# Kernel optimization log

Hardware: AMD Instinct MI355X
Metric: run time of the kernel (lower is better)

The kernel has to match this reference:

```python
import jax, jax.numpy as jnp
import numpy as np

D_MODEL = 256
SELF_NHEAD = 8
ATT_NHEAD = 8
DFF = 1024
H2D, W2D = 40, 40
MAX_DIS = 7
WS = 2 * MAX_DIS + 1  # 15x15 local window
LOCAL_DIL = 1
GN_GROUPS = 32
EPS = 1e-5


def _ln(x, g, b):
    m = jnp.mean(x, -1, keepdims=True)
    v = jnp.var(x, -1, keepdims=True)
    return (x - m) * jax.lax.rsqrt(v + EPS) * g + b


def _mha_core(q, k, v, nh):
    # q,k,v: (L, B, C); Q scaled by 1/sqrt(head_dim) as in AOT MultiheadAttention
    Lq, B, C = q.shape
    hd = C // nh
    qh = (q / jnp.asarray(hd ** 0.5, q.dtype)).reshape(Lq, B, nh, hd).transpose(1, 2, 0, 3)
    kh = k.reshape(-1, B, nh, hd).transpose(1, 2, 0, 3)
    vh = v.reshape(-1, B, nh, hd).transpose(1, 2, 0, 3)
    attn = jax.nn.softmax(jnp.einsum('bhqd,bhkd->bhqk', qh, kh), axis=-1)
    o = jnp.einsum('bhqk,bhkd->bhqd', attn, vh)
    return o.transpose(2, 0, 1, 3).reshape(Lq, B, C)


def _unfold(x, ws, dil):
    # x: (N, C, H, W) -> (N, C, ws*ws, H, W) local windows (zero-padded)
    n, c, h, w = x.shape
    p = (ws // 2) * dil
    pat = jax.lax.conv_general_dilated_patches(
        x, (ws, ws), (1, 1), [(p, p), (p, p)], rhs_dilation=(dil, dil))
    return pat.reshape(n, c, ws * ws, h, w)


def _local_attn(q2, k2, v2, nh, ws, dil):
    # q2,k2,v2: (B, C, H, W); windowed attention over (2*max_dis+1)^2 neighborhood
    b, c, h, w = q2.shape
    hd = c // nh
    qh = (q2 / jnp.asarray(hd ** 0.5, q2.dtype)).reshape(b, nh, hd, h * w)
    uk = _unfold(k2, ws, dil).reshape(b, nh, hd, ws * ws, h * w)
    uv = _unfold(v2, ws, dil).reshape(b, nh, hd, ws * ws, h * w)
    valid = _unfold(jnp.ones((1, 1, h, w), q2.dtype), ws, dil).reshape(1, 1, ws * ws, h * w) > 0.5
    logits = jnp.einsum('bhdn,bhdwn->bhwn', qh, uk)
    logits = jnp.where(valid, logits, jnp.asarray(-1e9, logits.dtype))
    attn = jax.nn.softmax(logits, axis=2)
    o = jnp.einsum('bhwn,bhdwn->bhdn', attn, uv)
    return o.reshape(b, c, h * w).transpose(2, 0, 1)  # (HW, B, C)


def _seq_to_2d(x, h, w):
    l, b, c = x.shape
    return x.reshape(h, w, b, c).transpose(2, 3, 0, 1)  # (B, C, h, w)


def _block(tgt, curr_id_emb, self_pos,
           ln1_g, ln1_b, sa_wq, sa_bq, sa_wk, sa_bk, sa_wv, sa_bv, sa_wo, sa_bo,
           ln2_g, ln2_b, w_qv, b_qv, w_id, b_id, lt_wo, lt_bo, st_wo, st_bo,
           ln3_g, ln3_b, w1, b1, gn_g, gn_b, dw_k, w2, b2):
    h, w = H2D, W2D
    # --- self attention (global_dilation == 1) ---
    _t = _ln(tgt, ln1_g, ln1_b)
    qk_in = _t + self_pos
    q_ = qk_in @ sa_wq.T + sa_bq
    k_ = qk_in @ sa_wk.T + sa_bk
    v_ = _t @ sa_wv.T + sa_bv
    tgt2 = _mha_core(q_, k_, v_, SELF_NHEAD) @ sa_wo.T + sa_bo
    tgt = tgt + tgt2
    # --- QV projection + ID-gated KV fusion ---
    _t = _ln(tgt, ln2_g, ln2_b)
    qv = _t @ w_qv.T + b_qv
    curr_Q = qv[..., :D_MODEL]  # curr_K == curr_Q
    curr_V = qv[..., D_MODEL:]
    id_kv = curr_id_emb @ w_id.T + b_id
    id_k = id_kv[..., :ATT_NHEAD]
    id_v = id_kv[..., ATT_NHEAD:]
    L, B, C = curr_Q.shape
    hd = C // ATT_NHEAD
    global_K = (curr_Q.reshape(L, B, ATT_NHEAD, hd) * (1.0 + jnp.tanh(id_k))[..., None]).reshape(L, B, C)
    global_V = curr_V + id_v
    # --- long-term (global) attention, no input linear ---
    tgt2 = _mha_core(curr_Q, global_K, global_V, ATT_NHEAD) @ lt_wo.T + lt_bo
    # --- short-term (local windowed) attention ---
    lq = _seq_to_2d(curr_Q, h, w)
    lk = _seq_to_2d(global_K, h, w)
    lv = _seq_to_2d(global_V, h, w)
    tgt3 = _local_attn(lq, lk, lv, ATT_NHEAD, WS, LOCAL_DIL) @ st_wo.T + st_bo
    tgt = tgt + tgt2 + tgt3
    # --- FFN with GN + GELU + depthwise 5x5 conv (GNActDWConv2d) ---
    _t = _ln(tgt, ln3_g, ln3_b)
    x = _t @ w1.T + b1  # (L, B, DFF)
    x2 = _seq_to_2d(x, h, w)  # (B, DFF, h, w)
    xr = x2.reshape(B, GN_GROUPS, DFF // GN_GROUPS, h, w)
    m = xr.mean((2, 3, 4), keepdims=True)
    va = xr.var((2, 3, 4), keepdims=True)
    x2 = ((xr - m) * jax.lax.rsqrt(va + EPS)).reshape(B, DFF, h, w)
    x2 = x2 * gn_g[None, :, None, None] + gn_b[None, :, None, None]
    x2 = jax.nn.gelu(x2, approximate=False)
    x2 = jax.lax.conv_general_dilated(
        x2, dw_k, (1, 1), [(2, 2), (2, 2)], feature_group_count=DFF,
        dimension_numbers=('NCHW', 'OIHW', 'NCHW'))
    x = x2.reshape(B, DFF, h * w).transpose(2, 0, 1)
    tgt2 = x @ w2.T + b2
    return tgt + tgt2


def setup_inputs() -> dict:
    key = jax.random.key(0)
    ks = jax.random.split(key, 40)
    L = H2D * W2D
    B = 1
    C = D_MODEL
    w = lambda k, s: jax.random.normal(k, s, jnp.float32) * 0.02
    inp = {
        'tgt': jax.random.normal(ks[0], (L, B, C), jnp.float32),
        'curr_id_emb': jax.random.normal(ks[1], (L, B, C), jnp.float32),
        'self_pos': jax.random.normal(ks[2], (L, B, C), jnp.float32),
        'ln1_g': jnp.ones((C,), jnp.float32), 'ln1_b': jnp.zeros((C,), jnp.float32),
        'sa_wq': w(ks[3], (C, C)), 'sa_bq': jnp.zeros((C,), jnp.float32),
        'sa_wk': w(ks[4], (C, C)), 'sa_bk': jnp.zeros((C,), jnp.float32),
        'sa_wv': w(ks[5], (C, C)), 'sa_bv': jnp.zeros((C,), jnp.float32),
        'sa_wo': w(ks[6], (C, C)), 'sa_bo': jnp.zeros((C,), jnp.float32),
        'ln2_g': jnp.ones((C,), jnp.float32), 'ln2_b': jnp.zeros((C,), jnp.float32),
        'w_qv': w(ks[7], (2 * C, C)), 'b_qv': jnp.zeros((2 * C,), jnp.float32),
        'w_id': w(ks[8], (C + ATT_NHEAD, C)), 'b_id': jnp.zeros((C + ATT_NHEAD,), jnp.float32),
        'lt_wo': w(ks[9], (C, C)), 'lt_bo': jnp.zeros((C,), jnp.float32),
        'st_wo': w(ks[10], (C, C)), 'st_bo': jnp.zeros((C,), jnp.float32),
        'ln3_g': jnp.ones((C,), jnp.float32), 'ln3_b': jnp.zeros((C,), jnp.float32),
        'w1': w(ks[11], (DFF, C)), 'b1': jnp.zeros((DFF,), jnp.float32),
        'gn_g': jnp.ones((DFF,), jnp.float32), 'gn_b': jnp.zeros((DFF,), jnp.float32),
        'dw_k': w(ks[12], (DFF, 1, 5, 5)),
        'w2': w(ks[13], (C, DFF)), 'b2': jnp.zeros((C,), jnp.float32),
    }
    return inp


def reference(tgt, curr_id_emb, self_pos,
              ln1_g, ln1_b, sa_wq, sa_bq, sa_wk, sa_bk, sa_wv, sa_bv, sa_wo, sa_bo,
              ln2_g, ln2_b, w_qv, b_qv, w_id, b_id, lt_wo, lt_bo, st_wo, st_bo,
              ln3_g, ln3_b, w1, b1, gn_g, gn_b, dw_k, w2, b2):
    return _block(tgt, curr_id_emb, self_pos,
                  ln1_g, ln1_b, sa_wq, sa_bq, sa_wk, sa_bk, sa_wv, sa_bv, sa_wo, sa_bo,
                  ln2_g, ln2_b, w_qv, b_qv, w_id, b_id, lt_wo, lt_bo, st_wo, st_bo,
                  ln3_g, ln3_b, w1, b1, gn_g, gn_b, dw_k, w2, b2)
```

## Files before the change

### kernel.cpp

```cpp
#include <hip/hip_runtime.h>
#include <math.h>

#define L_SEQ 1600
#define CDIM 256
#define NH 8
#define HD 32
#define GRID_H 40
#define GRID_W 40
#define DFF_ 1024
#define SCALE_QK 0.17677669529663687f

typedef __attribute__((ext_vector_type(8))) short short8;
typedef __attribute__((ext_vector_type(4))) float f32x4;

__device__ __forceinline__ float waveReduceSum(float v) {
#pragma unroll
    for (int off = 32; off > 0; off >>= 1) v += __shfl_down(v, off, 64);
    return v;
}
__device__ __forceinline__ float blockReduceSum(float v, float* sh4) {
    v = waveReduceSum(v);
    int lane = threadIdx.x & 63, wid = threadIdx.x >> 6;
    __syncthreads();
    if (lane == 0) sh4[wid] = v;
    __syncthreads();
    return sh4[0] + sh4[1] + sh4[2] + sh4[3];
}

__device__ __forceinline__ unsigned short f2bf(float x) {
    union { float f; unsigned u; } v; v.f = x;
    unsigned r = (v.u + 0x7FFFu + ((v.u >> 16) & 1u)) >> 16;
    return (unsigned short)r;
}
__device__ __forceinline__ unsigned pkbf(float lo, float hi) {
    return (unsigned)f2bf(lo) | ((unsigned)f2bf(hi) << 16);
}

__global__ __launch_bounds__(256) void ln_kernel(const float* __restrict__ x,
                                                 const float* __restrict__ g,
                                                 const float* __restrict__ b,
                                                 const float* __restrict__ addin,
                                                 float* __restrict__ out,
                                                 float* __restrict__ out2) {
    __shared__ float sh4[4];
    int row = blockIdx.x;
    int c = threadIdx.x;
    float v = x[row * CDIM + c];
    float mean = blockReduceSum(v, sh4) * (1.0f / CDIM);
    float d = v - mean;
    float var = blockReduceSum(d * d, sh4) * (1.0f / CDIM);
    float y = d * rsqrtf(var + 1e-5f) * g[c] + b[c];
    out[row * CDIM + c] = y;
    if (out2) out2[row * CDIM + c] = y + addin[row * CDIM + c];
}

struct GJob {
    const float* A; const float* W; const float* bias; const float* res;
    float* C; int N; int K;
};

__global__ __launch_bounds__(256) void gemm_mfma(GJob j0, GJob j1, GJob j2) {
    GJob j = j0;
    if (blockIdx.z == 1) j = j1;
    else if (blockIdx.z == 2) j = j2;
    const float* __restrict__ A = j.A;
    const float* __restrict__ W = j.W;
    const float* bias = j.bias;
    const float* res = j.res;
    float* __restrict__ C = j.C;
    int N = j.N, K = j.K;

    __shared__ unsigned short Al[2][4][64][8];
    __shared__ unsigned short Bl[2][4][64][8];
    int tid = threadIdx.x;
    int bm = blockIdx.y * 64, bn = blockIdx.x * 64;
    if (bn >= N) return;
    int lane = tid & 63, wave = tid >> 6;
    int wr = wave >> 1, wc = wave & 1;

    int srow = tid >> 3;
    int q = tid & 7;
    int e0 = (q & 1) * 4;

    f32x4 acc[2][2] = {};
    int nsteps = K >> 5;

    float4 ra[2], rb[2];
    {
#pragma unroll
        for (int r = 0; r < 2; ++r) {
            int row = srow + 32 * r;
            ra[r] = *(const float4*)(A + (bm + row) * K + 4 * q);
            int n = bn + row;
            rb[r] = (n < N) ? *(const float4*)(W + n * K + 4 * q)
                            : make_float4(0.f, 0.f, 0.f, 0.f);
        }
#pragma unroll
        for (int r = 0; r < 2; ++r) {
            int row = srow + 32 * r;
            int frag = (row >> 4), l = (row & 15) + 16 * (q >> 1);
            *(uint2*)&Al[0][frag][l][e0] = make_uint2(pkbf(ra[r].x, ra[r].y), pkbf(ra[r].z, ra[r].w));
            *(uint2*)&Bl[0][frag][l][e0] = make_uint2(pkbf(rb[r].x, rb[r].y), pkbf(rb[r].z, rb[r].w));
        }
    }
    __syncthreads();

    for (int s = 0; s < nsteps; ++s) {
        bool more = (s + 1) < nsteps;
        if (more) {
            int k0 = (s + 1) << 5;
#pragma unroll
            for (int r = 0; r < 2; ++r) {
                int row = srow + 32 * r;
                ra[r] = *(const float4*)(A + (bm + row) * K + k0 + 4 * q);
                int n = bn + row;
                rb[r] = (n < N) ? *(const float4*)(W + n * K + k0 + 4 * q)
                                : make_float4(0.f, 0.f, 0.f, 0.f);
            }
        }
        {
            int buf = s & 1;
            short8 af[2], bfr[2];
#pragma unroll
            for (int i = 0; i < 2; ++i) {
                af[i] = *(const short8*)&Al[buf][2 * wr + i][lane][0];
                bfr[i] = *(const short8*)&Bl[buf][2 * wc + i][lane][0];
            }
#pragma unroll
            for (int i = 0; i < 2; ++i)
#pragma unroll
                for (int jj = 0; jj < 2; ++jj)
                    acc[i][jj] = __builtin_amdgcn_mfma_f32_16x16x32_bf16(af[i], bfr[jj], acc[i][jj], 0, 0, 0);
        }
        if (more) {
            int buf = (s + 1) & 1;
#pragma unroll
            for (int r = 0; r < 2; ++r) {
                int row = srow + 32 * r;
                int frag = (row >> 4), l = (row & 15) + 16 * (q >> 1);
                *(uint2*)&Al[buf][frag][l][e0] = make_uint2(pkbf(ra[r].x, ra[r].y), pkbf(ra[r].z, ra[r].w));
                *(uint2*)&Bl[buf][frag][l][e0] = make_uint2(pkbf(rb[r].x, rb[r].y), pkbf(rb[r].z, rb[r].w));
            }
        }
        __syncthreads();
    }

#pragma unroll
    for (int jj = 0; jj < 2; ++jj) {
        int col = bn + wc * 32 + jj * 16 + (lane & 15);
        if (col >= N) continue;
        float bv = bias ? bias[col] : 0.f;
#pragma unroll
        for (int i = 0; i < 2; ++i) {
            int rbase = bm + wr * 32 + i * 16 + ((lane >> 4) << 2);
#pragma unroll
            for (int r = 0; r < 4; ++r) {
                int row = rbase + r;
                float v = acc[i][jj][r] + bv;
                if (res) v += res[row * N + col];
                C[row * N + col] = v;
            }
        }
    }
}

#define QBLK 32
#define KTJ 128
__global__ __launch_bounds__(256) void mha_mfma(const float* __restrict__ Q,
                                                const float* __restrict__ K,
                                                const float* __restrict__ V,
                                                float* __restrict__ O, int ldo) {
    __shared__ unsigned short Kl[8][64][8];
    __shared__ unsigned short Vl[4][2][64][12];
    __shared__ float mred[4][2][16];
    __shared__ float lred[4][2][16];
    __shared__ float Osh[3][2][2][64][4];
    int h = blockIdx.y;
    int qbase = blockIdx.x * QBLK;
    int tid = threadIdx.x;
    int w = tid >> 6, lane = tid & 63;
    int g = lane >> 4, c = lane & 15;

    short8 qfrag[2];
#pragma unroll
    for (int qt = 0; qt < 2; ++qt) {
        const float* qp = Q + (qbase + qt * 16 + c) * CDIM + h * HD + g * 8;
        float4 f0 = *(const float4*)qp;
        float4 f1 = *(const float4*)(qp + 4);
        short8 s;
        s[0] = (short)f2bf(f0.x * SCALE_QK); s[1] = (short)f2bf(f0.y * SCALE_QK);
        s[2] = (short)f2bf(f0.z * SCALE_QK); s[3] = (short)f2bf(f0.w * SCALE_QK);
        s[4] = (short)f2bf(f1.x * SCALE_QK); s[5] = (short)f2bf(f1.y * SCALE_QK);
        s[6] = (short)f2bf(f1.z * SCALE_QK); s[7] = (short)f2bf(f1.w * SCALE_QK);
        qfrag[qt] = s;
    }

    float m[2] = { -INFINITY, -INFINITY };
    float l[2] = { 0.f, 0.f };
    f32x4 acc_o[2][2] = {};

    int jrow = tid >> 1;
    int dhalf = (tid & 1) * 16;
    int vjq = tid >> 3;
    int vdq = tid & 7;
    int vjr = 4 * vjq;
    int vd0 = 4 * vdq;
    int vjc = vjr >> 5, vdt = vd0 >> 4, vjg = (vjr & 31) >> 3, ve0 = vjr & 7;

    int src_lo = 16 * ((2 * g) & 3) + c;
    int src_hi = 16 * ((2 * g + 1) & 3) + c;
    bool hisel = (g >= 2);

    for (int t = 0; t < L_SEQ; t += KTJ) {
        {
            int jj = t + jrow;
            float4 f0, f1, f2, f3;
            if (jj < L_SEQ) {
                const float4* kp = (const float4*)(K + jj * CDIM + h * HD + dhalf);
                f0 = kp[0]; f1 = kp[1]; f2 = kp[2]; f3 = kp[3];
            } else {
                f0 = f1 = f2 = f3 = make_float4(0.f, 0.f, 0.f, 0.f);
            }
            int jt = jrow >> 4;
            int laneA = (jrow & 15) + dhalf * 2;
            short8 s0, s1;
            s0[0]=f2bf(f0.x); s0[1]=f2bf(f0.y); s0[2]=f2bf(f0.z); s0[3]=f2bf(f0.w);
            s0[4]=f2bf(f1.x); s0[5]=f2bf(f1.y); s0[6]=f2bf(f1.z); s0[7]=f2bf(f1.w);
            s1[0]=f2bf(f2.x); s1[1]=f2bf(f2.y); s1[2]=f2bf(f2.z); s1[3]=f2bf(f2.w);
            s1[4]=f2bf(f3.x); s1[5]=f2bf(f3.y); s1[6]=f2bf(f3.z); s1[7]=f2bf(f3.w);
            *(short8*)&Kl[jt][laneA][0] = s0;
            *(short8*)&Kl[jt][laneA + 16][0] = s1;
        }
        {
            float4 r0, r1, r2, r3;
            int j0 = t + vjr;
            const float* vb = V + h * HD + vd0;
            r0 = (j0 + 0 < L_SEQ) ? *(const float4*)(vb + (j0 + 0) * CDIM) : make_float4(0,0,0,0);
            r1 = (j0 + 1 < L_SEQ) ? *(const float4*)(vb + (j0 + 1) * CDIM) : make_float4(0,0,0,0);
            r2 = (j0 + 2 < L_SEQ) ? *(const float4*)(vb + (j0 + 2) * CDIM) : make_float4(0,0,0,0);
            r3 = (j0 + 3 < L_SEQ) ? *(const float4*)(vb + (j0 + 3) * CDIM) : make_float4(0,0,0,0);
            float col[4][4] = {
                { r0.x, r1.x, r2.x, r3.x },
                { r0.y, r1.y, r2.y, r3.y },
                { r0.z, r1.z, r2.z, r3.z },
                { r0.w, r1.w, r2.w, r3.w } };
#pragma unroll
            for (int dd = 0; dd < 4; ++dd) {
                int laneV = ((vd0 + dd) & 15) + 16 * vjg;
                uint2 pk;
                pk.x = pkbf(col[dd][0], col[dd][1]);
                pk.y = pkbf(col[dd][2], col[dd][3]);
                *(uint2*)&Vl[vjc][vdt][laneV][ve0] = pk;
            }
        }
        __syncthreads();

        bool alive = (t + 32 * w) < L_SEQ;
        if (alive) {
            short8 kf0 = *(const short8*)&Kl[2 * w][lane][0];
            short8 kf1 = *(const short8*)&Kl[2 * w + 1][lane][0];
            f32x4 zero = { 0.f, 0.f, 0.f, 0.f };
            f32x4 s[2][2];
            s[0][0] = __builtin_amdgcn_mfma_f32_16x16x32_bf16(kf0, qfrag[0], zero, 0, 0, 0);
            s[0][1] = __builtin_amdgcn_mfma_f32_16x16x32_bf16(kf0, qfrag[1], zero, 0, 0, 0);
            s[1][0] = __builtin_amdgcn_mfma_f32_16x16x32_bf16(kf1, qfrag[0], zero, 0, 0, 0);
            s[1][1] = __builtin_amdgcn_mfma_f32_16x16x32_bf16(kf1, qfrag[1], zero, 0, 0, 0);

            short8 pfrag[2];
#pragma unroll
            for (int qt = 0; qt < 2; ++qt) {
                float mx = s[0][qt][0];
                mx = fmaxf(mx, s[0][qt][1]); mx = fmaxf(mx, s[0][qt][2]); mx = fmaxf(mx, s[0][qt][3]);
                mx = fmaxf(mx, s[1][qt][0]); mx = fmaxf(mx, s[1][qt][1]);
                mx = fmaxf(mx, s[1][qt][2]); mx = fmaxf(mx, s[1][qt][3]);
                mx = fmaxf(mx, __shfl_xor(mx, 16, 64));
                mx = fmaxf(mx, __shfl_xor(mx, 32, 64));
                float nm = fmaxf(m[qt], mx);
                float alpha = __expf(m[qt] - nm);
                m[qt] = nm;
                float p00 = __expf(s[0][qt][0] - nm), p01 = __expf(s[0][qt][1] - nm);
                float p02 = __expf(s[0][qt][2] - nm), p03 = __expf(s[0][qt][3] - nm);
                float p10 = __expf(s[1][qt][0] - nm), p11 = __expf(s[1][qt][1] - nm);
                float p12 = __expf(s[1][qt][2] - nm), p13 = __expf(s[1][qt][3] - nm);
                float ts = ((p00 + p01) + (p02 + p03)) + ((p10 + p11) + (p12 + p13));
                ts += __shfl_xor(ts, 16, 64);
                ts += __shfl_xor(ts, 32, 64);
                l[qt] = l[qt] * alpha + ts;
#pragma unroll
                for (int dt = 0; dt < 2; ++dt) {
                    acc_o[dt][qt][0] *= alpha; acc_o[dt][qt][1] *= alpha;
                    acc_o[dt][qt][2] *= alpha; acc_o[dt][qt][3] *= alpha;
                }
                unsigned w00 = pkbf(p00, p01), w01 = pkbf(p02, p03);
                unsigned w10 = pkbf(p10, p11), w11 = pkbf(p12, p13);
                unsigned a0 = __shfl(w00, src_lo, 64);
                unsigned a1 = __shfl(w10, src_lo, 64);
                unsigned b0 = __shfl(w01, src_lo, 64);
                unsigned b1 = __shfl(w11, src_lo, 64);
                unsigned c0 = __shfl(w00, src_hi, 64);
                unsigned c1 = __shfl(w10, src_hi, 64);
                unsigned d0 = __shfl(w01, src_hi, 64);
                unsigned d1 = __shfl(w11, src_hi, 64);
                union { short8 s8; unsigned u[4]; } P;
                P.u[0] = hisel ? a1 : a0;
                P.u[1] = hisel ? b1 : b0;
                P.u[2] = hisel ? c1 : c0;
                P.u[3] = hisel ? d1 : d0;
                pfrag[qt] = P.s8;
            }

            union { short8 s8; uint2 v[2]; } vf0u, vf1u;
            vf0u.v[0] = *(const uint2*)&Vl[w][0][lane][0];
            vf0u.v[1] = *(const uint2*)&Vl[w][0][lane][4];
            vf1u.v[0] = *(const uint2*)&Vl[w][1][lane][0];
            vf1u.v[1] = *(const uint2*)&Vl[w][1][lane][4];
            acc_o[0][0] = __builtin_amdgcn_mfma_f32_16x16x32_bf16(vf0u.s8, pfrag[0], acc_o[0][0], 0, 0, 0);
            acc_o[0][1] = __builtin_amdgcn_mfma_f32_16x16x32_bf16(vf0u.s8, pfrag[1], acc_o[0][1], 0, 0, 0);
            acc_o[1][0] = __builtin_amdgcn_mfma_f32_16x16x32_bf16(vf1u.s8, pfrag[0], acc_o[1][0], 0, 0, 0);
            acc_o[1][1] = __builtin_amdgcn_mfma_f32_16x16x32_bf16(vf1u.s8, pfrag[1], acc_o[1][1], 0, 0, 0);
        }
        __syncthreads();
    }

    if (g == 0) {
#pragma unroll
        for (int qt = 0; qt < 2; ++qt) { mred[w][qt][c] = m[qt]; lred[w][qt][c] = l[qt]; }
    }
    if (w > 0) {
#pragma unroll
        for (int dt = 0; dt < 2; ++dt)
#pragma unroll
            for (int qt = 0; qt < 2; ++qt)
                *(f32x4*)&Osh[w - 1][dt][qt][lane][0] = acc_o[dt][qt];
    }
    __syncthreads();
    if (w == 0) {
#pragma unroll
        for (int qt = 0; qt < 2; ++qt) {
            float m0_ = mred[0][qt][c], m1_ = mred[1][qt][c];
            float m2_ = mred[2][qt][c], m3_ = mred[3][qt][c];
            float M = fmaxf(fmaxf(m0_, m1_), fmaxf(m2_, m3_));
            float a0 = __expf(m0_ - M), a1 = __expf(m1_ - M);
            float a2 = __expf(m2_ - M), a3 = __expf(m3_ - M);
            float L = a0 * lred[0][qt][c] + a1 * lred[1][qt][c]
                    + a2 * lred[2][qt][c] + a3 * lred[3][qt][c];
            float inv = 1.f / L;
#pragma unroll
            for (int dt = 0; dt < 2; ++dt) {
                f32x4 o1 = *(const f32x4*)&Osh[0][dt][qt][lane][0];
                f32x4 o2 = *(const f32x4*)&Osh[1][dt][qt][lane][0];
                f32x4 o3 = *(const f32x4*)&Osh[2][dt][qt][lane][0];
                float4 r;
                r.x = (acc_o[dt][qt][0] * a0 + o1[0] * a1 + o2[0] * a2 + o3[0] * a3) * inv;
                r.y = (acc_o[dt][qt][1] * a0 + o1[1] * a1 + o2[1] * a2 + o3[1] * a3) * inv;
                r.z = (acc_o[dt][qt][2] * a0 + o1[2] * a1 + o2[2] * a2 + o3[2] * a3) * inv;
                r.w = (acc_o[dt][qt][3] * a0 + o1[3] * a1 + o2[3] * a2 + o3[3] * a3) * inv;
                *(float4*)(O + (qbase + qt * 16 + c) * ldo + h * HD + dt * 16 + 4 * g) = r;
            }
        }
    }
}

__global__ __launch_bounds__(256, 1) void local_mfma(const float* __restrict__ Q,
                                                     const float* __restrict__ K,
                                                     const float* __restrict__ V,
                                                     float* __restrict__ O, int ldo) {
    __shared__ unsigned short Kp[768 * 40];
    __shared__ unsigned short Vt[32 * 776];
    __shared__ float mred[4][3][16];
    __shared__ float lred[4][3][16];
    __shared__ float Osh[3][2][3][64][4];
    int y = blockIdx.x, h = blockIdx.y;
    int tid = threadIdx.x;
    int w = tid >> 6, lane = tid & 63;
    int g = lane >> 4, c = lane & 15;

#pragma unroll 4
    for (int rep = 0; rep < 24; ++rep) {
        int idx = rep * 256 + tid;
        int key = idx >> 3, dq = idx & 7;
        int ky = key / 48;
        int xx = key - 48 * ky;
        int yy = y + ky - 7;
        bool ok = (xx < 40) && (yy >= 0) && (yy < 40);
        float4 fk = make_float4(0.f, 0.f, 0.f, 0.f);
        float4 fv = make_float4(0.f, 0.f, 0.f, 0.f);
        if (ok) {
            int pos = (yy * 40 + xx) * CDIM + h * HD + 4 * dq;
            fk = *(const float4*)(K + pos);
            fv = *(const float4*)(V + pos);
        }
        *(uint2*)&Kp[key * 40 + 4 * dq] = make_uint2(pkbf(fk.x, fk.y), pkbf(fk.z, fk.w));
        int vb = (4 * dq) * 776 + key;
        Vt[vb] = f2bf(fv.x);
        Vt[vb + 776] = f2bf(fv.y);
        Vt[vb + 1552] = f2bf(fv.z);
        Vt[vb + 2328] = f2bf(fv.w);
    }

    short8 qfrag[3];
#pragma unroll
    for (int qt = 0; qt < 3; ++qt) {
        short8 s = { 0, 0, 0, 0, 0, 0, 0, 0 };
        int qx = qt * 16 + c;
        if (qx < 40) {
            const float* qp = Q + (y * 40 + qx) * CDIM + h * HD + g * 8;
            float4 f0 = *(const float4*)qp;
            float4 f1 = *(const float4*)(qp + 4);
            s[0] = (short)f2bf(f0.x * SCALE_QK); s[1] = (short)f2bf(f0.y * SCALE_QK);
            s[2] = (short)f2bf(f0.z * SCALE_QK); s[3] = (short)f2bf(f0.w * SCALE_QK);
            s[4] = (short)f2bf(f1.x * SCALE_QK); s[5] = (short)f2bf(f1.y * SCALE_QK);
            s[6] = (short)f2bf(f1.z * SCALE_QK); s[7] = (short)f2bf(f1.w * SCALE_QK);
        }
        qfrag[qt] = s;
    }
    __syncthreads();

    f32x4 sfr[12][3];
    const f32x4 zf = { 0.f, 0.f, 0.f, 0.f };
#pragma unroll
    for (int i = 0; i < 12; ++i) {
        int ky = 4 * w + i / 3;
        int fx = i % 3;
        short8 kf = *(const short8*)&Kp[(ky * 48 + fx * 16 + c) * 40 + 8 * g];
#pragma unroll
        for (int qt = 0; qt < 3; ++qt)
            sfr[i][qt] = __builtin_amdgcn_mfma_f32_16x16x32_bf16(kf, qfrag[qt], zf, 0, 0, 0);
    }

    float mw[3] = { -1e30f, -1e30f, -1e30f };
#pragma unroll
    for (int i = 0; i < 12; ++i) {
        int ky = 4 * w + i / 3, fx = i % 3;
        int yy = y + ky - 7;
        bool rowok = (yy >= 0) && (yy < 40);
        int xxb = fx * 16 + 4 * g;
#pragma unroll
        for (int qt = 0; qt < 3; ++qt) {
            int qx = qt * 16 + c;
#pragma unroll
            for (int r = 0; r < 4; ++r) {
                int xx = xxb + r;
                int dd = xx - qx;
                bool ok = rowok && (xx < 40) && (dd <= 7) && (dd >= -7);
                float v = ok ? sfr[i][qt][r] : -1e9f;
                sfr[i][qt][r] = v;
                mw[qt] = fmaxf(mw[qt], v);
            }
        }
    }
#pragma unroll
    for (int qt = 0; qt < 3; ++qt) {
        mw[qt] = fmaxf(mw[qt], __shfl_xor(mw[qt], 16, 64));
        mw[qt] = fmaxf(mw[qt], __shfl_xor(mw[qt], 32, 64));
    }
    if (lane < 16) {
#pragma unroll
        for (int qt = 0; qt < 3; ++qt) mred[w][qt][lane] = mw[qt];
    }
    __syncthreads();
    float M[3];
#pragma unroll
    for (int qt = 0; qt < 3; ++qt)
        M[qt] = fmaxf(fmaxf(mred[0][qt][c], mred[1][qt][c]),
                      fmaxf(mred[2][qt][c], mred[3][qt][c]));

    float lsum[3] = { 0.f, 0.f, 0.f };
    f32x4 acc_o[2][3] = {};
    int src_lo = 16 * ((2 * g) & 3) + c;
    int src_hi = 16 * ((2 * g + 1) & 3) + c;
    bool hisel = (g >= 2);
#pragma unroll
    for (int chk = 0; chk < 6; ++chk) {
        short8 pfrag[3];
#pragma unroll
        for (int qt = 0; qt < 3; ++qt) {
            float p00 = __expf(sfr[2 * chk][qt][0] - M[qt]);
            float p01 = __expf(sfr[2 * chk][qt][1] - M[qt]);
            float p02 = __expf(sfr[2 * chk][qt][2] - M[qt]);
            float p03 = __expf(sfr[2 * chk][qt][3] - M[qt]);
            float p10 = __expf(sfr[2 * chk + 1][qt][0] - M[qt]);
            float p11 = __expf(sfr[2 * chk + 1][qt][1] - M[qt]);
            float p12 = __expf(sfr[2 * chk + 1][qt][2] - M[qt]);
            float p13 = __expf(sfr[2 * chk + 1][qt][3] - M[qt]);
            lsum[qt] += ((p00 + p01) + (p02 + p03)) + ((p10 + p11) + (p12 + p13));
            unsigned w00 = pkbf(p00, p01), w01 = pkbf(p02, p03);
            unsigned w10 = pkbf(p10, p11), w11 = pkbf(p12, p13);
            unsigned a0 = __shfl(w00, src_lo, 64);
            unsigned a1 = __shfl(w10, src_lo, 64);
            unsigned b0 = __shfl(w01, src_lo, 64);
            unsigned b1 = __shfl(w11, src_lo, 64);
            unsigned c0 = __shfl(w00, src_hi, 64);
            unsigned c1 = __shfl(w10, src_hi, 64);
            unsigned d0 = __shfl(w01, src_hi, 64);
            unsigned d1 = __shfl(w11, src_hi, 64);
            union { short8 s8; unsigned u[4]; } P;
            P.u[0] = hisel ? a1 : a0;
            P.u[1] = hisel ? b1 : b0;
            P.u[2] = hisel ? c1 : c0;
            P.u[3] = hisel ? d1 : d0;
            pfrag[qt] = P.s8;
        }
        int jb = 32 * (6 * w + chk);
        short8 vf0 = *(const short8*)&Vt[c * 776 + jb + 8 * g];
        short8 vf1 = *(const short8*)&Vt[(16 + c) * 776 + jb + 8 * g];
#pragma unroll
        for (int qt = 0; qt < 3; ++qt) {
            acc_o[0][qt] = __builtin_amdgcn_mfma_f32_16x16x32_bf16(vf0, pfrag[qt], acc_o[0][qt], 0, 0, 0);
            acc_o[1][qt] = __builtin_amdgcn_mfma_f32_16x16x32_bf16(vf1, pfrag[qt], acc_o[1][qt], 0, 0, 0);
        }
    }

#pragma unroll
    for (int qt = 0; qt < 3; ++qt) {
        lsum[qt] += __shfl_xor(lsum[qt], 16, 64);
        lsum[qt] += __shfl_xor(lsum[qt], 32, 64);
    }
    if (lane < 16) {
#pragma unroll
        for (int qt = 0; qt < 3; ++qt) lred[w][qt][lane] = lsum[qt];
    }
    if (w > 0) {
#pragma unroll
        for (int dt = 0; dt < 2; ++dt)
#pragma unroll
            for (int qt = 0; qt < 3; ++qt)
                *(f32x4*)&Osh[w - 1][dt][qt][lane][0] = acc_o[dt][qt];
    }
    __syncthreads();
    if (w == 0) {
#pragma unroll
        for (int qt = 0; qt < 3; ++qt) {
            int qx = qt * 16 + c;
            if (qx >= 40) continue;
            float L = (lred[0][qt][c] + lred[1][qt][c]) + (lred[2][qt][c] + lred[3][qt][c]);
            float inv = 1.f / L;
#pragma unroll
            for (int dt = 0; dt < 2; ++dt) {
                f32x4 o1 = *(const f32x4*)&Osh[0][dt][qt][lane][0];
                f32x4 o2 = *(const f32x4*)&Osh[1][dt][qt][lane][0];
                f32x4 o3 = *(const f32x4*)&Osh[2][dt][qt][lane][0];
                float4 r;
                r.x = (acc_o[dt][qt][0] + o1[0] + o2[0] + o3[0]) * inv;
                r.y = (acc_o[dt][qt][1] + o1[1] + o2[1] + o3[1]) * inv;
                r.z = (acc_o[dt][qt][2] + o1[2] + o2[2] + o3[2]) * inv;
                r.w = (acc_o[dt][qt][3] + o1[3] + o2[3] + o3[3]) * inv;
                *(float4*)(O + (y * 40 + qx) * ldo + h * HD + dt * 16 + 4 * g) = r;
            }
        }
    }
}

__global__ __launch_bounds__(256) void make_qkv_kernel(const float* __restrict__ qv,
                                                       const float* __restrict__ idkv,
                                                       float* __restrict__ Qc,
                                                       float* __restrict__ gK,
                                                       float* __restrict__ gV) {
    int idx = blockIdx.x * 256 + threadIdx.x;
    if (idx >= L_SEQ * CDIM) return;
    int l = idx >> 8, c = idx & 255;
    int h = c >> 5;
    float q = qv[l * 512 + c];
    Qc[idx] = q;
    gK[idx] = q * (1.f + tanhf(idkv[l * 264 + h]));
    gV[idx] = qv[l * 512 + 256 + c] + idkv[l * 264 + 8 + c];
}

__global__ __launch_bounds__(256) void prep_ltst(const float* __restrict__ lt_wo,
                                                 const float* __restrict__ lt_bo,
                                                 const float* __restrict__ st_wo,
                                                 const float* __restrict__ st_bo,
                                                 float* __restrict__ wcat,
                                                 float* __restrict__ bsum) {
    int idx = blockIdx.x * 256 + threadIdx.x;
    int n = idx >> 8, k = idx & 255;
    wcat[n * 512 + k] = lt_wo[idx];
    wcat[n * 512 + 256 + k] = st_wo[idx];
    if (idx < 256) bsum[idx] = lt_bo[idx] + st_bo[idx];
}

__global__ __launch_bounds__(256) void gn_partial(const float* __restrict__ X,
                                                  float* __restrict__ gstat) {
    __shared__ float sh4[4];
    int g = blockIdx.x, chunk = blockIdx.y;
    int base = g * 32;
    float s = 0.f, s2 = 0.f;
    for (int i = threadIdx.x; i < 200 * 32; i += 256) {
        int l = chunk * 200 + (i >> 5), c = i & 31;
        float v = X[l * DFF_ + base + c];
        s += v;
        s2 += v * v;
    }
    s = blockReduceSum(s, sh4);
    s2 = blockReduceSum(s2, sh4);
    if (threadIdx.x == 0) {
        gstat[g * 8 + chunk] = s;
        gstat[256 + g * 8 + chunk] = s2;
    }
}

__global__ __launch_bounds__(256) void gn_apply(const float* __restrict__ X,
                                                const float* __restrict__ gstat,
                                                const float* __restrict__ g,
                                                const float* __restrict__ b,
                                                float* __restrict__ Y) {
    int idx = blockIdx.x * 256 + threadIdx.x;
    int e4 = idx * 4;
    int c = e4 & 1023;
    int grp = c >> 5;
    float s = 0.f, s2 = 0.f;
#pragma unroll
    for (int i = 0; i < 8; ++i) {
        s += gstat[grp * 8 + i];
        s2 += gstat[256 + grp * 8 + i];
    }
    const float invn = 1.0f / 51200.f;
    float mean = s * invn;
    float rs = rsqrtf(s2 * invn - mean * mean + 1e-5f);
    float4 v = *(const float4*)(X + e4);
    float4 gg = *(const float4*)(g + c);
    float4 bb = *(const float4*)(b + c);
    float4 r;
    float y0 = (v.x - mean) * rs * gg.x + bb.x;
    float y1 = (v.y - mean) * rs * gg.y + bb.y;
    float y2 = (v.z - mean) * rs * gg.z + bb.z;
    float y3 = (v.w - mean) * rs * gg.w + bb.w;
    r.x = 0.5f * y0 * (1.0f + erff(y0 * 0.70710678118654752f));
    r.y = 0.5f * y1 * (1.0f + erff(y1 * 0.70710678118654752f));
    r.z = 0.5f * y2 * (1.0f + erff(y2 * 0.70710678118654752f));
    r.w = 0.5f * y3 * (1.0f + erff(y3 * 0.70710678118654752f));
    *(float4*)(Y + e4) = r;
}

__global__ __launch_bounds__(256) void dwk_transpose(const float* __restrict__ Kw,
                                                     float* __restrict__ Kt) {
    int idx = blockIdx.x * 256 + threadIdx.x;
    if (idx >= 25 * DFF_) return;
    int k = idx >> 10, c = idx & 1023;
    Kt[idx] = Kw[c * 25 + k];
}

__global__ __launch_bounds__(256) void dwconv_v2(const float* __restrict__ X,
                                                 const float* __restrict__ Kt,
                                                 float* __restrict__ Y) {
    int l = blockIdx.x;
    int c4 = threadIdx.x * 4;
    int y = l / GRID_W, x = l - y * GRID_W;
    float4 acc = make_float4(0.f, 0.f, 0.f, 0.f);
    if (y >= 2 && y < GRID_H - 2 && x >= 2 && x < GRID_W - 2) {
#pragma unroll
        for (int ky = 0; ky < 5; ++ky) {
#pragma unroll
            for (int kx = 0; kx < 5; ++kx) {
                float4 xv = *(const float4*)(X + ((y + ky - 2) * GRID_W + x + kx - 2) * DFF_ + c4);
                float4 wv = *(const float4*)(Kt + (ky * 5 + kx) * DFF_ + c4);
                acc.x += xv.x * wv.x; acc.y += xv.y * wv.y;
                acc.z += xv.z * wv.z; acc.w += xv.w * wv.w;
            }
        }
    } else {
#pragma unroll
        for (int ky = 0; ky < 5; ++ky) {
            int yy = y + ky - 2;
            if (yy < 0 || yy >= GRID_H) continue;
#pragma unroll
            for (int kx = 0; kx < 5; ++kx) {
                int xx = x + kx - 2;
                if (xx < 0 || xx >= GRID_W) continue;
                float4 xv = *(const float4*)(X + (yy * GRID_W + xx) * DFF_ + c4);
                float4 wv = *(const float4*)(Kt + (ky * 5 + kx) * DFF_ + c4);
                acc.x += xv.x * wv.x; acc.y += xv.y * wv.y;
                acc.z += xv.z * wv.z; acc.w += xv.w * wv.w;
            }
        }
    }
    *(float4*)(Y + l * DFF_ + c4) = acc;
}

extern "C" void kernel_launch(void* const* d_in, const int* in_sizes, int n_in,
                              void* d_out, int out_size, void* d_ws, size_t ws_size,
                              hipStream_t stream) {
    (void)in_sizes; (void)n_in; (void)out_size; (void)ws_size;
    const float* tgt = (const float*)d_in[0];
    const float* curr_id_emb = (const float*)d_in[1];
    const float* self_pos = (const float*)d_in[2];
    const float* ln1_g = (const float*)d_in[3];
    const float* ln1_b = (const float*)d_in[4];
    const float* sa_wq = (const float*)d_in[5];
    const float* sa_bq = (const float*)d_in[6];
    const float* sa_wk = (const float*)d_in[7];
    const float* sa_bk = (const float*)d_in[8];
    const float* sa_wv = (const float*)d_in[9];
    const float* sa_bv = (const float*)d_in[10];
    const float* sa_wo = (const float*)d_in[11];
    const float* sa_bo = (const float*)d_in[12];
    const float* ln2_g = (const float*)d_in[13];
    const float* ln2_b = (const float*)d_in[14];
    const float* w_qv = (const float*)d_in[15];
    const float* b_qv = (const float*)d_in[16];
    const float* w_id = (const float*)d_in[17];
    const float* b_id = (const float*)d_in[18];
    const float* lt_wo = (const float*)d_in[19];
    const float* lt_bo = (const float*)d_in[20];
    const float* st_wo = (const float*)d_in[21];
    const float* st_bo = (const float*)d_in[22];
    const float* ln3_g = (const float*)d_in[23];
    const float* ln3_b = (const float*)d_in[24];
    const float* w1 = (const float*)d_in[25];
    const float* b1 = (const float*)d_in[26];
    const float* gn_g = (const float*)d_in[27];
    const float* gn_b = (const float*)d_in[28];
    const float* dw_k = (const float*)d_in[29];
    const float* w2 = (const float*)d_in[30];
    const float* b2 = (const float*)d_in[31];
    float* out = (float*)d_out;

    float* ws = (float*)d_ws;
    const int LC = L_SEQ * CDIM;
    float* bufA = ws;
    float* bufB = bufA + LC;
    float* bufC = bufB + LC;
    float* bufD = bufC + LC;
    float* bufE = bufD + LC;
    float* bufG = bufE + LC;
    float* bufFW = bufG + LC;
    float* bufH = bufFW + L_SEQ * 512;
    float* bufI = bufH + L_SEQ * 512;
    float* bufX = bufI + L_SEQ * 264;
    float* bufY = bufX + L_SEQ * DFF_;
    float* bufZ = bufY + L_SEQ * DFF_;
    float* bufW = bufZ + L_SEQ * DFF_;
    float* wcat = bufW + 25 * DFF_;
    float* bsum = wcat + 256 * 512;

    dim3 blk(256);
    dim3 mhaGrid(L_SEQ / QBLK, NH);
    auto J = [](const float* A, const float* W, const float* bias, const float* res,
                float* C, int N, int K) {
        GJob j; j.A = A; j.W = W; j.bias = bias; j.res = res; j.C = C; j.N = N; j.K = K;
        return j;
    };

    dwk_transpose<<<100, blk, 0, stream>>>(dw_k, bufW);
    prep_ltst<<<256, blk, 0, stream>>>(lt_wo, lt_bo, st_wo, st_bo, wcat, bsum);
    ln_kernel<<<L_SEQ, blk, 0, stream>>>(tgt, ln1_g, ln1_b, self_pos, bufA, bufB);
    {
        GJob jq = J(bufB, sa_wq, sa_bq, nullptr, bufC, CDIM, CDIM);
        GJob jk = J(bufB, sa_wk, sa_bk, nullptr, bufD, CDIM, CDIM);
        GJob jv = J(bufA, sa_wv, sa_bv, nullptr, bufE, CDIM, CDIM);
        gemm_mfma<<<dim3(4, 25, 3), blk, 0, stream>>>(jq, jk, jv);
    }
    mha_mfma<<<mhaGrid, blk, 0, stream>>>(bufC, bufD, bufE, bufFW, CDIM);
    {
        GJob jo = J(bufFW, sa_wo, sa_bo, tgt, bufG, CDIM, CDIM);
        gemm_mfma<<<dim3(4, 25, 1), blk, 0, stream>>>(jo, jo, jo);
    }
    ln_kernel<<<L_SEQ, blk, 0, stream>>>(bufG, ln2_g, ln2_b, nullptr, bufA, nullptr);
    {
        GJob jqv = J(bufA, w_qv, b_qv, nullptr, bufH, 512, CDIM);
        GJob jid = J(curr_id_emb, w_id, b_id, nullptr, bufI, 264, CDIM);
        gemm_mfma<<<dim3(8, 25, 2), blk, 0, stream>>>(jqv, jid, jid);
    }
    make_qkv_kernel<<<L_SEQ, blk, 0, stream>>>(bufH, bufI, bufC, bufD, bufE);
    mha_mfma<<<mhaGrid, blk, 0, stream>>>(bufC, bufD, bufE, bufFW, 512);
    local_mfma<<<dim3(GRID_H, NH), blk, 0, stream>>>(bufC, bufD, bufE, bufFW + 256, 512);
    {
        GJob jm = J(bufFW, wcat, bsum, bufG, bufB, CDIM, 512);
        gemm_mfma<<<dim3(4, 25, 1), blk, 0, stream>>>(jm, jm, jm);
    }
    ln_kernel<<<L_SEQ, blk, 0, stream>>>(bufB, ln3_g, ln3_b, nullptr, bufA, nullptr);
    {
        GJob jw1 = J(bufA, w1, b1, nullptr, bufX, DFF_, CDIM);
        gemm_mfma<<<dim3(16, 25, 1), blk, 0, stream>>>(jw1, jw1, jw1);
    }
    gn_partial<<<dim3(32, 8), blk, 0, stream>>>(bufX, bufH);
    gn_apply<<<L_SEQ, blk, 0, stream>>>(bufX, bufH, gn_g, gn_b, bufY);
    dwconv_v2<<<L_SEQ, blk, 0, stream>>>(bufY, bufW, bufZ);
    {
        GJob jw2 = J(bufZ, w2, b2, bufB, out, CDIM, DFF_);
        gemm_mfma<<<dim3(4, 25, 1), blk, 0, stream>>>(jw2, jw2, jw2);
    }
}
```

Baseline: 348.5 us.

## Fuse ID-gating into attention loads, double query block, merge prep kernels

Removes the make_qkv kernel: the global and local attention kernels now read Q/K/V straight from the fused qv buffer with strides and apply the tanh ID gate to K and the ID add to V while staging into LDS. The MHA query block grows from 32 to 64 rows, so each K/V tile is reused across four 16-row query tiles and the grid is halved. The dwconv kernel transpose is folded into the lt/st weight-prep kernel, saving a launch. The risks are extra tanh work recomputed per block during K staging, higher register pressure, and fewer blocks (200) for occupancy.

Result: slower. 387.8 us (+11.3%).

```diff
diff --git a/kernel.cpp b/kernel.cpp
--- a/kernel.cpp
+++ b/kernel.cpp
@@ -164,27 +164,28 @@
     }
 }
 
-#define QBLK 32
+#define QBLK 64
 #define KTJ 128
-__global__ __launch_bounds__(256) void mha_mfma(const float* __restrict__ Q,
-                                                const float* __restrict__ K,
-                                                const float* __restrict__ V,
+__global__ __launch_bounds__(256) void mha_mfma(const float* __restrict__ Q, int ldq,
+                                                const float* __restrict__ K, int ldk,
+                                                const float* __restrict__ V, int ldv,
+                                                const float* __restrict__ idkv,
                                                 float* __restrict__ O, int ldo) {
     __shared__ unsigned short Kl[8][64][8];
     __shared__ unsigned short Vl[4][2][64][12];
-    __shared__ float mred[4][2][16];
-    __shared__ float lred[4][2][16];
-    __shared__ float Osh[3][2][2][64][4];
+    __shared__ float mred[4][4][16];
+    __shared__ float lred[4][4][16];
+    __shared__ float Osh[3][2][4][64][4];
     int h = blockIdx.y;
     int qbase = blockIdx.x * QBLK;
     int tid = threadIdx.x;
     int w = tid >> 6, lane = tid & 63;
     int g = lane >> 4, c = lane & 15;
 
-    short8 qfrag[2];
-#pragma unroll
-    for (int qt = 0; qt < 2; ++qt) {
-        const float* qp = Q + (qbase + qt * 16 + c) * CDIM + h * HD + g * 8;
+    short8 qfrag[4];
+#pragma unroll
+    for (int qt = 0; qt < 4; ++qt) {
+        const float* qp = Q + (qbase + qt * 16 + c) * ldq + h * HD + g * 8;
         float4 f0 = *(const float4*)qp;
         float4 f1 = *(const float4*)(qp + 4);
         short8 s;
@@ -195,9 +196,9 @@
         qfrag[qt] = s;
     }
 
-    float m[2] = { -INFINITY, -INFINITY };
-    float l[2] = { 0.f, 0.f };
-    f32x4 acc_o[2][2] = {};
+    float m[4] = { -INFINITY, -INFINITY, -INFINITY, -INFINITY };
+    float l[4] = { 0.f, 0.f, 0.f, 0.f };
+    f32x4 acc_o[2][4] = {};
 
     int jrow = tid >> 1;
     int dhalf = (tid & 1) * 16;
@@ -216,8 +217,15 @@
             int jj = t + jrow;
             float4 f0, f1, f2, f3;
             if (jj < L_SEQ) {
-                const float4* kp = (const float4*)(K + jj * CDIM + h * HD + dhalf);
+                const float4* kp = (const float4*)(K + jj * ldk + h * HD + dhalf);
                 f0 = kp[0]; f1 = kp[1]; f2 = kp[2]; f3 = kp[3];
+                if (idkv) {
+                    float gt = 1.f + tanhf(idkv[jj * 264 + h]);
+                    f0.x *= gt; f0.y *= gt; f0.z *= gt; f0.w *= gt;
+                    f1.x *= gt; f1.y *= gt; f1.z *= gt; f1.w *= gt;
+                    f2.x *= gt; f2.y *= gt; f2.z *= gt; f2.w *= gt;
+                    f3.x *= gt; f3.y *= gt; f3.z *= gt; f3.w *= gt;
+                }
             } else {
                 f0 = f1 = f2 = f3 = make_float4(0.f, 0.f, 0.f, 0.f);
             }
@@ -232,18 +240,27 @@
             *(short8*)&Kl[jt][laneA + 16][0] = s1;
         }
         {
-            float4 r0, r1, r2, r3;
+            float4 rr[4];
             int j0 = t + vjr;
-            const float* vb = V + h * HD + vd0;
-            r0 = (j0 + 0 < L_SEQ) ? *(const float4*)(vb + (j0 + 0) * CDIM) : make_float4(0,0,0,0);
-            r1 = (j0 + 1 < L_SEQ) ? *(const float4*)(vb + (j0 + 1) * CDIM) : make_float4(0,0,0,0);
-            r2 = (j0 + 2 < L_SEQ) ? *(const float4*)(vb + (j0 + 2) * CDIM) : make_float4(0,0,0,0);
-            r3 = (j0 + 3 < L_SEQ) ? *(const float4*)(vb + (j0 + 3) * CDIM) : make_float4(0,0,0,0);
+#pragma unroll
+            for (int r = 0; r < 4; ++r) {
+                int jj = j0 + r;
+                if (jj < L_SEQ) {
+                    float4 fv = *(const float4*)(V + jj * ldv + h * HD + vd0);
+                    if (idkv) {
+                        float4 av = *(const float4*)(idkv + jj * 264 + 8 + h * HD + vd0);
+                        fv.x += av.x; fv.y += av.y; fv.z += av.z; fv.w += av.w;
+                    }
+                    rr[r] = fv;
+                } else {
+                    rr[r] = make_float4(0.f, 0.f, 0.f, 0.f);
+                }
+            }
             float col[4][4] = {
-                { r0.x, r1.x, r2.x, r3.x },
-                { r0.y, r1.y, r2.y, r3.y },
-                { r0.z, r1.z, r2.z, r3.z },
-                { r0.w, r1.w, r2.w, r3.w } };
+                { rr[0].x, rr[1].x, rr[2].x, rr[3].x },
+                { rr[0].y, rr[1].y, rr[2].y, rr[3].y },
+                { rr[0].z, rr[1].z, rr[2].z, rr[3].z },
+                { rr[0].w, rr[1].w, rr[2].w, rr[3].w } };
 #pragma unroll
             for (int dd = 0; dd < 4; ++dd) {
                 int laneV = ((vd0 + dd) & 15) + 16 * vjg;
@@ -260,15 +277,16 @@
             short8 kf0 = *(const short8*)&Kl[2 * w][lane][0];
             short8 kf1 = *(const short8*)&Kl[2 * w + 1][lane][0];
             f32x4 zero = { 0.f, 0.f, 0.f, 0.f };
-            f32x4 s[2][2];
-            s[0][0] = __builtin_amdgcn_mfma_f32_16x16x32_bf16(kf0, qfrag[0], zero, 0, 0, 0);
-            s[0][1] = __builtin_amdgcn_mfma_f32_16x16x32_bf16(kf0, qfrag[1], zero, 0, 0, 0);
-            s[1][0] = __builtin_amdgcn_mfma_f32_16x16x32_bf16(kf1, qfrag[0], zero, 0, 0, 0);
-            s[1][1] = __builtin_amdgcn_mfma_f32_16x16x32_bf16(kf1, qfrag[1], zero, 0, 0, 0);
-
-            short8 pfrag[2];
-#pragma unroll
-            for (int qt = 0; qt < 2; ++qt) {
+            f32x4 s[2][4];
+#pragma unroll
+            for (int qt = 0; qt < 4; ++qt) {
+                s[0][qt] = __builtin_amdgcn_mfma_f32_16x16x32_bf16(kf0, qfrag[qt], zero, 0, 0, 0);
+                s[1][qt] = __builtin_amdgcn_mfma_f32_16x16x32_bf16(kf1, qfrag[qt], zero, 0, 0, 0);
+            }
+
+            short8 pfrag[4];
+#pragma unroll
+            for (int qt = 0; qt < 4; ++qt) {
                 float mx = s[0][qt][0];
                 mx = fmaxf(mx, s[0][qt][1]); mx = fmaxf(mx, s[0][qt][2]); mx = fmaxf(mx, s[0][qt][3]);
                 mx = fmaxf(mx, s[1][qt][0]); mx = fmaxf(mx, s[1][qt][1]);
@@ -314,29 +332,30 @@
             vf0u.v[1] = *(const uint2*)&Vl[w][0][lane][4];
             vf1u.v[0] = *(const uint2*)&Vl[w][1][lane][0];
             vf1u.v[1] = *(const uint2*)&Vl[w][1][lane][4];
-            acc_o[0][0] = __builtin_amdgcn_mfma_f32_16x16x32_bf16(vf0u.s8, pfrag[0], acc_o[0][0], 0, 0, 0);
-            acc_o[0][1] = __builtin_amdgcn_mfma_f32_16x16x32_bf16(vf0u.s8, pfrag[1], acc_o[0][1], 0, 0, 0);
-            acc_o[1][0] = __builtin_amdgcn_mfma_f32_16x16x32_bf16(vf1u.s8, pfrag[0], acc_o[1][0], 0, 0, 0);
-            acc_o[1][1] = __builtin_amdgcn_mfma_f32_16x16x32_bf16(vf1u.s8, pfrag[1], acc_o[1][1], 0, 0, 0);
+#pragma unroll
+            for (int qt = 0; qt < 4; ++qt) {
+                acc_o[0][qt] = __builtin_amdgcn_mfma_f32_16x16x32_bf16(vf0u.s8, pfrag[qt], acc_o[0][qt], 0, 0, 0);
+                acc_o[1][qt] = __builtin_amdgcn_mfma_f32_16x16x32_bf16(vf1u.s8, pfrag[qt], acc_o[1][qt], 0, 0, 0);
+            }
         }
         __syncthreads();
     }
 
     if (g == 0) {
 #pragma unroll
-        for (int qt = 0; qt < 2; ++qt) { mred[w][qt][c] = m[qt]; lred[w][qt][c] = l[qt]; }
+        for (int qt = 0; qt < 4; ++qt) { mred[w][qt][c] = m[qt]; lred[w][qt][c] = l[qt]; }
     }
     if (w > 0) {
 #pragma unroll
         for (int dt = 0; dt < 2; ++dt)
 #pragma unroll
-            for (int qt = 0; qt < 2; ++qt)
+            for (int qt = 0; qt < 4; ++qt)
                 *(f32x4*)&Osh[w - 1][dt][qt][lane][0] = acc_o[dt][qt];
     }
     __syncthreads();
     if (w == 0) {
 #pragma unroll
-        for (int qt = 0; qt < 2; ++qt) {
+        for (int qt = 0; qt < 4; ++qt) {
             float m0_ = mred[0][qt][c], m1_ = mred[1][qt][c];
             float m2_ = mred[2][qt][c], m3_ = mred[3][qt][c];
             float M = fmaxf(fmaxf(m0_, m1_), fmaxf(m2_, m3_));
@@ -361,9 +380,10 @@
     }
 }
 
-__global__ __launch_bounds__(256, 1) void local_mfma(const float* __restrict__ Q,
-                                                     const float* __restrict__ K,
-                                                     const float* __restrict__ V,
+__global__ __launch_bounds__(256, 1) void local_mfma(const float* __restrict__ Q, int ldq,
+                                                     const float* __restrict__ K, int ldk,
+                                                     const float* __restrict__ V, int ldv,
+                                                     const float* __restrict__ idkv,
                                                      float* __restrict__ O, int ldo) {
     __shared__ unsigned short Kp[768 * 40];
     __shared__ unsigned short Vt[32 * 776];
@@ -386,9 +406,15 @@
         float4 fk = make_float4(0.f, 0.f, 0.f, 0.f);
         float4 fv = make_float4(0.f, 0.f, 0.f, 0.f);
         if (ok) {
-            int pos = (yy * 40 + xx) * CDIM + h * HD + 4 * dq;
-            fk = *(const float4*)(K + pos);
-            fv = *(const float4*)(V + pos);
+            int row = yy * 40 + xx;
+            fk = *(const float4*)(K + row * ldk + h * HD + 4 * dq);
+            fv = *(const float4*)(V + row * ldv + h * HD + 4 * dq);
+            if (idkv) {
+                float gt = 1.f + tanhf(idkv[row * 264 + h]);
+                fk.x *= gt; fk.y *= gt; fk.z *= gt; fk.w *= gt;
+                float4 av = *(const float4*)(idkv + row * 264 + 8 + h * HD + 4 * dq);
+                fv.x += av.x; fv.y += av.y; fv.z += av.z; fv.w += av.w;
+            }
         }
         *(uint2*)&Kp[key * 40 + 4 * dq] = make_uint2(pkbf(fk.x, fk.y), pkbf(fk.z, fk.w));
         int vb = (4 * dq) * 776 + key;
@@ -404,7 +430,7 @@
         short8 s = { 0, 0, 0, 0, 0, 0, 0, 0 };
         int qx = qt * 16 + c;
         if (qx < 40) {
-            const float* qp = Q + (y * 40 + qx) * CDIM + h * HD + g * 8;
+            const float* qp = Q + (y * 40 + qx) * ldq + h * HD + g * 8;
             float4 f0 = *(const float4*)qp;
             float4 f1 = *(const float4*)(qp + 4);
             s[0] = (short)f2bf(f0.x * SCALE_QK); s[1] = (short)f2bf(f0.y * SCALE_QK);
@@ -551,25 +577,12 @@
     }
 }
 
-__global__ __launch_bounds__(256) void make_qkv_kernel(const float* __restrict__ qv,
-                                                       const float* __restrict__ idkv,
-                                                       float* __restrict__ Qc,
-                                                       float* __restrict__ gK,
-                                                       float* __restrict__ gV) {
-    int idx = blockIdx.x * 256 + threadIdx.x;
-    if (idx >= L_SEQ * CDIM) return;
-    int l = idx >> 8, c = idx & 255;
-    int h = c >> 5;
-    float q = qv[l * 512 + c];
-    Qc[idx] = q;
-    gK[idx] = q * (1.f + tanhf(idkv[l * 264 + h]));
-    gV[idx] = qv[l * 512 + 256 + c] + idkv[l * 264 + 8 + c];
-}
-
-__global__ __launch_bounds__(256) void prep_ltst(const float* __restrict__ lt_wo,
+__global__ __launch_bounds__(256) void prep_misc(const float* __restrict__ Kw,
+                                                 const float* __restrict__ lt_wo,
                                                  const float* __restrict__ lt_bo,
                                                  const float* __restrict__ st_wo,
                                                  const float* __restrict__ st_bo,
+                                                 float* __restrict__ Kt,
                                                  float* __restrict__ wcat,
                                                  float* __restrict__ bsum) {
     int idx = blockIdx.x * 256 + threadIdx.x;
@@ -577,6 +590,10 @@
     wcat[n * 512 + k] = lt_wo[idx];
     wcat[n * 512 + 256 + k] = st_wo[idx];
     if (idx < 256) bsum[idx] = lt_bo[idx] + st_bo[idx];
+    if (idx < 25 * DFF_) {
+        int kk = idx >> 10, c = idx & 1023;
+        Kt[idx] = Kw[c * 25 + kk];
+    }
 }
 
 __global__ __launch_bounds__(256) void gn_partial(const float* __restrict__ X,
@@ -630,14 +647,6 @@
     r.z = 0.5f * y2 * (1.0f + erff(y2 * 0.70710678118654752f));
     r.w = 0.5f * y3 * (1.0f + erff(y3 * 0.70710678118654752f));
     *(float4*)(Y + e4) = r;
-}
-
-__global__ __launch_bounds__(256) void dwk_transpose(const float* __restrict__ Kw,
-                                                     float* __restrict__ Kt) {
-    int idx = blockIdx.x * 256 + threadIdx.x;
-    if (idx >= 25 * DFF_) return;
-    int k = idx >> 10, c = idx & 1023;
-    Kt[idx] = Kw[c * 25 + k];
 }
 
 __global__ __launch_bounds__(256) void dwconv_v2(const float* __restrict__ X,
@@ -741,8 +750,7 @@
         return j;
     };
 
-    dwk_transpose<<<100, blk, 0, stream>>>(dw_k, bufW);
-    prep_ltst<<<256, blk, 0, stream>>>(lt_wo, lt_bo, st_wo, st_bo, wcat, bsum);
+    prep_misc<<<256, blk, 0, stream>>>(dw_k, lt_wo, lt_bo, st_wo, st_bo, bufW, wcat, bsum);
     ln_kernel<<<L_SEQ, blk, 0, stream>>>(tgt, ln1_g, ln1_b, self_pos, bufA, bufB);
     {
         GJob jq = J(bufB, sa_wq, sa_bq, nullptr, bufC, CDIM, CDIM);
@@ -750,7 +758,7 @@
         GJob jv = J(bufA, sa_wv, sa_bv, nullptr, bufE, CDIM, CDIM);
         gemm_mfma<<<dim3(4, 25, 3), blk, 0, stream>>>(jq, jk, jv);
     }
-    mha_mfma<<<mhaGrid, blk, 0, stream>>>(bufC, bufD, bufE, bufFW, CDIM);
+    mha_mfma<<<mhaGrid, blk, 0, stream>>>(bufC, CDIM, bufD, CDIM, bufE, CDIM, nullptr, bufFW, CDIM);
     {
         GJob jo = J(bufFW, sa_wo, sa_bo, tgt, bufG, CDIM, CDIM);
         gemm_mfma<<<dim3(4, 25, 1), blk, 0, stream>>>(jo, jo, jo);
@@ -761,9 +769,8 @@
         GJob jid = J(curr_id_emb, w_id, b_id, nullptr, bufI, 264, CDIM);
         gemm_mfma<<<dim3(8, 25, 2), blk, 0, stream>>>(jqv, jid, jid);
     }
-    make_qkv_kernel<<<L_SEQ, blk, 0, stream>>>(bufH, bufI, bufC, bufD, bufE);
-    mha_mfma<<<mhaGrid, blk, 0, stream>>>(bufC, bufD, bufE, bufFW, 512);
-    local_mfma<<<dim3(GRID_H, NH), blk, 0, stream>>>(bufC, bufD, bufE, bufFW + 256, 512);
+    mha_mfma<<<mhaGrid, blk, 0, stream>>>(bufH, 512, bufH, 512, bufH + 256, 512, bufI, bufFW, 512);
+    local_mfma<<<dim3(GRID_H, NH), blk, 0, stream>>>(bufH, 512, bufH, 512, bufH + 256, 512, bufI, bufFW + 256, 512);
     {
         GJob jm = J(bufFW, wcat, bsum, bufG, bufB, CDIM, 512);
         gemm_mfma<<<dim3(4, 25, 1), blk, 0, stream>>>(jm, jm, jm);
```
